# Performance work log

Measured on AMD Instinct MI355X. Metric: run time of the kernel, lower is better.

Reference implementation:

```python
import jax, jax.numpy as jnp
import numpy as np

N = 50000      # n_nodes
E = 800000     # n_edges (avg degree 16)
D_IN, D_HID, D_OUT = 128, 128, 64


def setup_inputs() -> dict:
    key = jax.random.key(0)
    k1, k2, k3, k4 = jax.random.split(key, 4)
    x = jax.random.normal(k1, (N, D_IN), jnp.float32)
    edge_index = jax.random.randint(k2, (2, E), 0, N, jnp.int32)
    # Glorot-style init for the two GCNConv linear weights
    W1 = jax.random.normal(k3, (D_IN, D_HID), jnp.float32) / np.sqrt(D_IN)
    W2 = jax.random.normal(k4, (D_HID, D_OUT), jnp.float32) / np.sqrt(D_HID)
    b1 = jnp.zeros((D_HID,), jnp.float32)
    b2 = jnp.zeros((D_OUT,), jnp.float32)
    return {"x": x, "edge_index": edge_index, "W1": W1, "b1": b1, "W2": W2, "b2": b2}


def _gcn_conv(x, W, b, src, dst):
    """PyG GCNConv: linear transform, then sym-normalized aggregation with self-loops."""
    h = x @ W                                   # [N, F_out]
    ones = jnp.ones((src.shape[0],), h.dtype)
    # degree includes the self-loop weight of 1
    deg = jax.ops.segment_sum(ones, dst, num_segments=N) + 1.0
    dinv = jax.lax.rsqrt(deg)                   # D^{-1/2}
    norm = dinv[src] * dinv[dst]                # per-edge normalization
    agg = jax.ops.segment_sum(h[src] * norm[:, None], dst, num_segments=N)
    # self-loop contribution: norm_ii = dinv_i^2
    return agg + h * (dinv * dinv)[:, None] + b


def reference(x, edge_index, W1, b1, W2, b2):
    src, dst = edge_index[0], edge_index[1]
    h = jax.nn.relu(_gcn_conv(x, W1, b1, src, dst))
    out = jax.nn.relu(_gcn_conv(h, W2, b2, src, dst))
    return out
```

## Files before the change

### kernel.cpp

```cpp
#include <hip/hip_runtime.h>

typedef unsigned short u16;
typedef __attribute__((ext_vector_type(8))) short short8;
typedef __attribute__((ext_vector_type(4))) float f32x4;

__device__ __forceinline__ float bflo(unsigned u) {
    union { unsigned u; float f; } v; v.u = u << 16; return v.f;
}
__device__ __forceinline__ float bfhi(unsigned u) {
    union { unsigned u; float f; } v; v.u = u & 0xFFFF0000u; return v.f;
}
__device__ __forceinline__ u16 f2bf(float f) {
    union { float f; unsigned u; } v; v.f = f;
    unsigned u = v.u;
    u += 0x7FFFu + ((u >> 16) & 1u);
    return (u16)(u >> 16);
}

__global__ void k1_gemm_deg(const void* __restrict__ Av, const void* __restrict__ W,
                            u16* __restrict__ out, int M, int GB,
                            const int* __restrict__ dst, int* __restrict__ cnt,
                            int* __restrict__ pos, int E, int* __restrict__ flag) {
    constexpr int NOUT = 128;
    int t = threadIdx.x;
    int bid = blockIdx.x;
    if (bid >= GB) {
        if (bid == GB) {
            __shared__ int c_s;
            if (t == 0) c_s = 0;
            __syncthreads();
            int c = 0;
            for (int i = t; i < 2048; i += 256) {
                int ex = (((const u16*)Av)[2 * i] >> 7) & 0xFF;
                c += (ex >= 160 || ex <= 80) ? 1 : 0;
            }
            atomicAdd(&c_s, c);
            __syncthreads();
            if (t == 0) *flag = (c_s > 64) ? 1 : 0;
        }
        int stride = (gridDim.x - GB) * 256;
        for (int e = (bid - GB) * 256 + t; e < E; e += stride)
            pos[e] = atomicAdd(&cnt[dst[e]], 1);
        return;
    }
    __shared__ int det;
    if (t == 0) det = 0;
    __syncthreads();
    {
        int ex = (((const u16*)Av)[2 * t] >> 7) & 0xFF;
        if (ex >= 160 || ex <= 80) atomicAdd(&det, 1);
    }
    __syncthreads();
    int fl = det > 8;

    __shared__ u16 Wt[NOUT][136];
    for (int idx = t; idx < NOUT * 128; idx += 256) {
        int k = idx / NOUT, n = idx % NOUT;
        Wt[n][k] = fl ? f2bf(((const float*)W)[idx]) : ((const u16*)W)[idx];
    }
    __syncthreads();
    int wave = t >> 6, lane = t & 63;
    int m0 = (bid * 4 + wave) * 16;
    if (m0 >= M) return;
    int q = lane >> 4;
    int mr = lane & 15;

    short8 a[4];
    if (fl) {
        const float* arow = (const float*)Av + (size_t)(m0 + mr) * 128 + q * 8;
#pragma unroll
        for (int c = 0; c < 4; c++) {
            f32x4 lo = *(const f32x4*)(arow + c * 32);
            f32x4 hi = *(const f32x4*)(arow + c * 32 + 4);
            a[c][0] = (short)f2bf(lo.x); a[c][1] = (short)f2bf(lo.y);
            a[c][2] = (short)f2bf(lo.z); a[c][3] = (short)f2bf(lo.w);
            a[c][4] = (short)f2bf(hi.x); a[c][5] = (short)f2bf(hi.y);
            a[c][6] = (short)f2bf(hi.z); a[c][7] = (short)f2bf(hi.w);
        }
    } else {
        const u16* arow = (const u16*)Av + (size_t)(m0 + mr) * 128 + q * 8;
#pragma unroll
        for (int c = 0; c < 4; c++) a[c] = *(const short8*)(arow + c * 32);
    }

    f32x4 acc[NOUT / 16];
#pragma unroll
    for (int tl = 0; tl < NOUT / 16; tl++) acc[tl] = (f32x4){0.f, 0.f, 0.f, 0.f};
#pragma unroll
    for (int c = 0; c < 4; c++) {
#pragma unroll
        for (int tl = 0; tl < NOUT / 16; tl++) {
            short8 b = *(const short8*)(&Wt[tl * 16 + mr][c * 32 + q * 8]);
            acc[tl] = __builtin_amdgcn_mfma_f32_16x16x32_bf16(a[c], b, acc[tl], 0, 0, 0);
        }
    }
    int rbase = m0 + q * 4;
#pragma unroll
    for (int tl = 0; tl < NOUT / 16; tl++) {
#pragma unroll
        for (int r = 0; r < 4; r++)
            out[(size_t)(rbase + r) * NOUT + tl * 16 + mr] = f2bf(acc[tl][r]);
    }
}

__global__ void k_scan_blocks(const int* __restrict__ cnt, int* __restrict__ rowp_p,
                              int* __restrict__ sums, int n) {
    __shared__ int s[256];
    int t = threadIdx.x;
    int i = blockIdx.x * 256 + t;
    int v = (i < n) ? cnt[i] : 0;
    s[t] = v;
    __syncthreads();
    for (int off = 1; off < 256; off <<= 1) {
        int add = (t >= off) ? s[t - off] : 0;
        __syncthreads();
        s[t] += add;
        __syncthreads();
    }
    if (i < n) rowp_p[i] = s[t] - v;
    if (t == 255) sums[blockIdx.x] = s[255];
}

__global__ void k_fin_fill(const int* __restrict__ rowp_p, int* __restrict__ rowp,
                           const int* __restrict__ sums, const int* __restrict__ cnt,
                           float* __restrict__ dinv, int n, int nb,
                           const int* __restrict__ src, const int* __restrict__ dst,
                           const int* __restrict__ pos, int* __restrict__ col, int E) {
    __shared__ int s[256];
    int t = threadIdx.x;
    int b = blockIdx.x;
    s[t] = sums[t];
    __syncthreads();
    for (int off = 1; off < 256; off <<= 1) {
        int add = (t >= off) ? s[t - off] : 0;
        __syncthreads();
        s[t] += add;
        __syncthreads();
    }
    __syncthreads();
    if (b < nb) {
        int prefix = (b == 0) ? 0 : s[b - 1];
        int i = b * 256 + t;
        if (i < n) {
            rowp[i] = rowp_p[i] + prefix;
            dinv[i] = rsqrtf((float)cnt[i] + 1.0f);
        }
        if (i == 0) rowp[n] = E;
    } else {
        int stride = (gridDim.x - nb) * 256;
        for (int e = (b - nb) * 256 + t; e < E; e += stride) {
            int d = dst[e];
            int tile = d >> 8;
            int prefix = (tile == 0) ? 0 : s[tile - 1];
            col[rowp_p[d] + prefix + pos[e]] = src[e];
        }
    }
}

template <int NOUT>
__global__ void k_gemm_plain(const u16* __restrict__ A, const void* __restrict__ W,
                             u16* __restrict__ out, int M, const int* __restrict__ flag) {
    int fl = *flag;
    __shared__ u16 Wt[NOUT][136];
    int t = threadIdx.x;
    for (int idx = t; idx < NOUT * 128; idx += 256) {
        int k = idx / NOUT, n = idx % NOUT;
        Wt[n][k] = fl ? f2bf(((const float*)W)[idx]) : ((const u16*)W)[idx];
    }
    __syncthreads();
    int wave = t >> 6, lane = t & 63;
    int m0 = ((int)blockIdx.x * 4 + wave) * 16;
    if (m0 >= M) return;
    int q = lane >> 4;
    int mr = lane & 15;

    const u16* arow = A + (size_t)(m0 + mr) * 128 + q * 8;
    short8 a[4];
#pragma unroll
    for (int c = 0; c < 4; c++) a[c] = *(const short8*)(arow + c * 32);

    f32x4 acc[NOUT / 16];
#pragma unroll
    for (int tl = 0; tl < NOUT / 16; tl++) acc[tl] = (f32x4){0.f, 0.f, 0.f, 0.f};
#pragma unroll
    for (int c = 0; c < 4; c++) {
#pragma unroll
        for (int tl = 0; tl < NOUT / 16; tl++) {
            short8 b = *(const short8*)(&Wt[tl * 16 + mr][c * 32 + q * 8]);
            acc[tl] = __builtin_amdgcn_mfma_f32_16x16x32_bf16(a[c], b, acc[tl], 0, 0, 0);
        }
    }
    int rbase = m0 + q * 4;
#pragma unroll
    for (int tl = 0; tl < NOUT / 16; tl++) {
#pragma unroll
        for (int r = 0; r < 4; r++)
            out[(size_t)(rbase + r) * NOUT + tl * 16 + mr] = f2bf(acc[tl][r]);
    }
}

template <int F>
__global__ void k_agg(const u16* __restrict__ g, const int* __restrict__ rowp,
                      const int* __restrict__ col, const float* __restrict__ dinv,
                      const void* __restrict__ biasv, u16* __restrict__ outh,
                      float* __restrict__ outf, const int* __restrict__ flag,
                      int outsel, int N, int E) {
    constexpr int LPR = F / 8;
    constexpr int EPW = 64 / LPR;
    int d = blockIdx.x * 4 + (threadIdx.x >> 6);
    if (d >= N) return;
    int lane = threadIdx.x & 63;
    int er = lane / LPR;
    int fo = (lane % LPR) * 8;

    int beg = rowp[d], end = rowp[d + 1];
    if (beg < 0) beg = 0;
    if (end > E) end = E;
    int deg = end - beg;

    float a0[8], a1[8];
#pragma unroll
    for (int j = 0; j < 8; j++) { a0[j] = 0.f; a1[j] = 0.f; }

    for (int base = 0; base < deg; base += 64) {
        int cnt = deg - base; if (cnt > 64) cnt = 64;
        int colv = 0;
        if (lane < cnt) {
            int s = col[beg + base + lane];
            colv = s < 0 ? 0 : (s >= N ? N - 1 : s);
        }
        int full = cnt / EPW;
        int i = 0;
        for (; i + 2 <= full; i += 2) {
            int s0 = __shfl(colv, i * EPW + er, 64);
            int s1 = __shfl(colv, (i + 1) * EPW + er, 64);
            float d0 = dinv[s0];
            float d1 = dinv[s1];
            uint4 v0 = *(const uint4*)(g + (size_t)s0 * F + fo);
            uint4 v1 = *(const uint4*)(g + (size_t)s1 * F + fo);
            a0[0] += d0 * bflo(v0.x); a0[1] += d0 * bfhi(v0.x);
            a0[2] += d0 * bflo(v0.y); a0[3] += d0 * bfhi(v0.y);
            a0[4] += d0 * bflo(v0.z); a0[5] += d0 * bfhi(v0.z);
            a0[6] += d0 * bflo(v0.w); a0[7] += d0 * bfhi(v0.w);
            a1[0] += d1 * bflo(v1.x); a1[1] += d1 * bfhi(v1.x);
            a1[2] += d1 * bflo(v1.y); a1[3] += d1 * bfhi(v1.y);
            a1[4] += d1 * bflo(v1.z); a1[5] += d1 * bfhi(v1.z);
            a1[6] += d1 * bflo(v1.w); a1[7] += d1 * bfhi(v1.w);
        }
        if (i < full) {
            int s0 = __shfl(colv, i * EPW + er, 64);
            float d0 = dinv[s0];
            uint4 v0 = *(const uint4*)(g + (size_t)s0 * F + fo);
            a0[0] += d0 * bflo(v0.x); a0[1] += d0 * bfhi(v0.x);
            a0[2] += d0 * bflo(v0.y); a0[3] += d0 * bfhi(v0.y);
            a0[4] += d0 * bflo(v0.z); a0[5] += d0 * bfhi(v0.z);
            a0[6] += d0 * bflo(v0.w); a0[7] += d0 * bfhi(v0.w);
            i++;
        }
        int rem = cnt - full * EPW;
        int s0 = __shfl(colv, (full * EPW + er) & 63, 64);
        float d0 = dinv[s0];
        if (er < rem) {
            uint4 v0 = *(const uint4*)(g + (size_t)s0 * F + fo);
            a0[0] += d0 * bflo(v0.x); a0[1] += d0 * bfhi(v0.x);
            a0[2] += d0 * bflo(v0.y); a0[3] += d0 * bfhi(v0.y);
            a0[4] += d0 * bflo(v0.z); a0[5] += d0 * bfhi(v0.z);
            a0[6] += d0 * bflo(v0.w); a0[7] += d0 * bfhi(v0.w);
        }
    }
#pragma unroll
    for (int j = 0; j < 8; j++) a0[j] += a1[j];
#pragma unroll
    for (int off = LPR; off < 64; off <<= 1) {
#pragma unroll
        for (int j = 0; j < 8; j++) a0[j] += __shfl_xor(a0[j], off, 64);
    }

    if (lane < LPR) {
        int fl = *flag;
        uint4 sv = *(const uint4*)(g + (size_t)d * F + fo);
        float bb[8];
        if (fl) {
            const float* bp = (const float*)biasv + fo;
            f32x4 blo = *(const f32x4*)bp;
            f32x4 bhi = *(const f32x4*)(bp + 4);
            bb[0] = blo.x; bb[1] = blo.y; bb[2] = blo.z; bb[3] = blo.w;
            bb[4] = bhi.x; bb[5] = bhi.y; bb[6] = bhi.z; bb[7] = bhi.w;
        } else {
            uint4 bv = *(const uint4*)((const u16*)biasv + fo);
            bb[0] = bflo(bv.x); bb[1] = bfhi(bv.x);
            bb[2] = bflo(bv.y); bb[3] = bfhi(bv.y);
            bb[4] = bflo(bv.z); bb[5] = bfhi(bv.z);
            bb[6] = bflo(bv.w); bb[7] = bfhi(bv.w);
        }
        float di = dinv[d];
        float sf[8] = { bflo(sv.x), bfhi(sv.x), bflo(sv.y), bfhi(sv.y),
                        bflo(sv.z), bfhi(sv.z), bflo(sv.w), bfhi(sv.w) };
        float r[8];
#pragma unroll
        for (int j = 0; j < 8; j++) {
            float v = di * (a0[j] + di * sf[j]) + bb[j];
            r[j] = v > 0.f ? v : 0.f;
        }
        size_t o = (size_t)d * F + fo;
        if (outsel && fl) {
            f32x4 w0 = {r[0], r[1], r[2], r[3]};
            f32x4 w1 = {r[4], r[5], r[6], r[7]};
            *(f32x4*)(outf + o) = w0;
            *(f32x4*)(outf + o + 4) = w1;
        } else {
            uint4 w;
            w.x = (unsigned)f2bf(r[0]) | ((unsigned)f2bf(r[1]) << 16);
            w.y = (unsigned)f2bf(r[2]) | ((unsigned)f2bf(r[3]) << 16);
            w.z = (unsigned)f2bf(r[4]) | ((unsigned)f2bf(r[5]) << 16);
            w.w = (unsigned)f2bf(r[6]) | ((unsigned)f2bf(r[7]) << 16);
            *(uint4*)(outh + o) = w;
        }
    }
}


extern "C" void kernel_launch(void* const* d_in, const int* in_sizes, int n_in,
                              void* d_out, int out_size, void* d_ws, size_t ws_size,
                              hipStream_t stream) {
    const int N = in_sizes[0] / 128;
    const int E = in_sizes[1] / 2;
    const int* ei = (const int*)d_in[1];
    const int* src = ei;
    const int* dst = ei + E;

    char* p = (char*)d_ws;
    auto alloc = [&](size_t b) { char* r = p; p += (b + 255) & ~(size_t)255; return r; };
    int*   flag   = (int*)alloc(256);
    int*   rowp   = (int*)alloc((size_t)(N + 1) * 4);
    int*   rowp_p = (int*)alloc((size_t)N * 4);
    float* dinv   = (float*)alloc((size_t)N * 4);
    int*   col    = (int*)alloc((size_t)E * 4);
    int*   cnt    = (int*)alloc((size_t)N * 4);
    int*   sums   = (int*)alloc(256 * 4);
    int*   pos    = (int*)alloc((size_t)E * 4);
    u16*   g1     = (u16*)alloc((size_t)N * 128 * 2);
    u16*   o1     = (u16*)alloc((size_t)N * 128 * 2);
    u16*   g2     = (u16*)alloc((size_t)N * 64 * 2);

    int nb = (N + 255) / 256;
    int GB = (N / 16 + 3) / 4;
    int DB = 782;
    int FB = 1024;
    int ab = (N + 3) / 4;

    hipMemsetAsync(cnt, 0, ((char*)sums - (char*)cnt) + 1024, stream);

    k1_gemm_deg<<<GB + DB, 256, 0, stream>>>(d_in[0], d_in[2], g1, N, GB,
                                             dst, cnt, pos, E, flag);
    k_scan_blocks<<<nb, 256, 0, stream>>>(cnt, rowp_p, sums, N);
    k_fin_fill<<<nb + FB, 256, 0, stream>>>(rowp_p, rowp, sums, cnt, dinv, N, nb,
                                            src, dst, pos, col, E);

    k_agg<128><<<ab, 256, 0, stream>>>(g1, rowp, col, dinv, d_in[3],
                                       o1, nullptr, flag, 0, N, E);
    k_gemm_plain<64><<<GB, 256, 0, stream>>>(o1, d_in[4], g2, N, flag);
    k_agg<64><<<ab, 256, 0, stream>>>(g2, rowp, col, dinv, d_in[5],
                                      (u16*)d_out, (float*)d_out, flag, 1, N, E);
}
```

Measured before the change: 212.1 us.

## Replace global atomic CSR build with per-block LDS histograms and chunked counting

Degree counting and CSR column fill now use per-block shared-memory histograms over node chunks instead of global atomics per edge. Each of 128 edge-slice blocks writes a u16 histogram, k_scan2 turns these into per-block offsets and degrees, and the fill kernel recomputes local ranks with LDS atomics. This removes contended global atomics and the pos array. In exchange each block rescans its edge slice once per node chunk, the 50KB LDS buffer is now also carried by the GEMM blocks and may lower their occupancy, and the scan reads a 128xN histogram.

```diff
diff --git a/kernel.cpp b/kernel.cpp
--- a/kernel.cpp
+++ b/kernel.cpp
@@ -17,15 +17,19 @@
     return (u16)(u >> 16);
 }
 
-__global__ void k1_gemm_deg(const void* __restrict__ Av, const void* __restrict__ W,
-                            u16* __restrict__ out, int M, int GB,
-                            const int* __restrict__ dst, int* __restrict__ cnt,
-                            int* __restrict__ pos, int E, int* __restrict__ flag) {
+#define CS 12500
+
+__global__ void k1_gemm_count(const void* __restrict__ Av, const void* __restrict__ W,
+                              u16* __restrict__ out, int M, int GB,
+                              const int* __restrict__ dst, u16* __restrict__ ghist,
+                              int E, int N, int ES, int* __restrict__ flag) {
     constexpr int NOUT = 128;
+    __shared__ __align__(16) char ldsbuf[50048];
     int t = threadIdx.x;
     int bid = blockIdx.x;
     if (bid >= GB) {
-        if (bid == GB) {
+        int b = bid - GB;
+        if (b == 0) {
             __shared__ int c_s;
             if (t == 0) c_s = 0;
             __syncthreads();
@@ -38,9 +42,22 @@
             __syncthreads();
             if (t == 0) *flag = (c_s > 64) ? 1 : 0;
         }
-        int stride = (gridDim.x - GB) * 256;
-        for (int e = (bid - GB) * 256 + t; e < E; e += stride)
-            pos[e] = atomicAdd(&cnt[dst[e]], 1);
+        unsigned* hist = (unsigned*)ldsbuf;
+        int e0 = b * ES;
+        int e1 = e0 + ES; if (e1 > E) e1 = E;
+        for (int lo = 0; lo < N; lo += CS) {
+            int len = N - lo; if (len > CS) len = CS;
+            __syncthreads();
+            for (int i = t; i < len; i += 256) hist[i] = 0;
+            __syncthreads();
+            for (int e = e0 + t; e < e1; e += 256) {
+                unsigned dd = (unsigned)(dst[e] - lo);
+                if (dd < (unsigned)len) atomicAdd(&hist[dd], 1u);
+            }
+            __syncthreads();
+            for (int i = t; i < len; i += 256)
+                ghist[(size_t)b * N + lo + i] = (u16)hist[i];
+        }
         return;
     }
     __shared__ int det;
@@ -53,7 +70,7 @@
     __syncthreads();
     int fl = det > 8;
 
-    __shared__ u16 Wt[NOUT][136];
+    u16 (*Wt)[136] = (u16(*)[136])ldsbuf;
     for (int idx = t; idx < NOUT * 128; idx += 256) {
         int k = idx / NOUT, n = idx % NOUT;
         Wt[n][k] = fl ? f2bf(((const float*)W)[idx]) : ((const u16*)W)[idx];
@@ -90,8 +107,8 @@
     for (int c = 0; c < 4; c++) {
 #pragma unroll
         for (int tl = 0; tl < NOUT / 16; tl++) {
-            short8 b = *(const short8*)(&Wt[tl * 16 + mr][c * 32 + q * 8]);
-            acc[tl] = __builtin_amdgcn_mfma_f32_16x16x32_bf16(a[c], b, acc[tl], 0, 0, 0);
+            short8 bb = *(const short8*)(&Wt[tl * 16 + mr][c * 32 + q * 8]);
+            acc[tl] = __builtin_amdgcn_mfma_f32_16x16x32_bf16(a[c], bb, acc[tl], 0, 0, 0);
         }
     }
     int rbase = m0 + q * 4;
@@ -103,13 +120,22 @@
     }
 }
 
-__global__ void k_scan_blocks(const int* __restrict__ cnt, int* __restrict__ rowp_p,
-                              int* __restrict__ sums, int n) {
+__global__ void k_scan2(u16* __restrict__ ghist, int* __restrict__ rowp_p,
+                        int* __restrict__ sums, float* __restrict__ dinv,
+                        int n, int NB) {
     __shared__ int s[256];
     int t = threadIdx.x;
     int i = blockIdx.x * 256 + t;
-    int v = (i < n) ? cnt[i] : 0;
-    s[t] = v;
+    int deg = 0;
+    if (i < n) {
+        for (int b = 0; b < NB; b++) {
+            size_t idx = (size_t)b * n + i;
+            int v = ghist[idx];
+            ghist[idx] = (u16)deg;
+            deg += v;
+        }
+    }
+    s[t] = deg;
     __syncthreads();
     for (int off = 1; off < 256; off <<= 1) {
         int add = (t >= off) ? s[t - off] : 0;
@@ -117,16 +143,20 @@
         s[t] += add;
         __syncthreads();
     }
-    if (i < n) rowp_p[i] = s[t] - v;
+    if (i < n) {
+        rowp_p[i] = s[t] - deg;
+        dinv[i] = rsqrtf((float)deg + 1.0f);
+    }
     if (t == 255) sums[blockIdx.x] = s[255];
 }
 
-__global__ void k_fin_fill(const int* __restrict__ rowp_p, int* __restrict__ rowp,
-                           const int* __restrict__ sums, const int* __restrict__ cnt,
-                           float* __restrict__ dinv, int n, int nb,
-                           const int* __restrict__ src, const int* __restrict__ dst,
-                           const int* __restrict__ pos, int* __restrict__ col, int E) {
+__global__ void k_fin_fill2(const int* __restrict__ rowp_p, int* __restrict__ rowp,
+                            const int* __restrict__ sums, int n, int nb,
+                            const int* __restrict__ src, const int* __restrict__ dst,
+                            const u16* __restrict__ ghist, int* __restrict__ col,
+                            int E, int N, int ES) {
     __shared__ int s[256];
+    __shared__ __align__(16) char ldsbuf[50048];
     int t = threadIdx.x;
     int b = blockIdx.x;
     s[t] = sums[t];
@@ -141,18 +171,28 @@
     if (b < nb) {
         int prefix = (b == 0) ? 0 : s[b - 1];
         int i = b * 256 + t;
-        if (i < n) {
-            rowp[i] = rowp_p[i] + prefix;
-            dinv[i] = rsqrtf((float)cnt[i] + 1.0f);
-        }
+        if (i < n) rowp[i] = rowp_p[i] + prefix;
         if (i == 0) rowp[n] = E;
     } else {
-        int stride = (gridDim.x - nb) * 256;
-        for (int e = (b - nb) * 256 + t; e < E; e += stride) {
-            int d = dst[e];
-            int tile = d >> 8;
-            int prefix = (tile == 0) ? 0 : s[tile - 1];
-            col[rowp_p[d] + prefix + pos[e]] = src[e];
+        int fb = b - nb;
+        unsigned* hist = (unsigned*)ldsbuf;
+        int e0 = fb * ES;
+        int e1 = e0 + ES; if (e1 > E) e1 = E;
+        for (int lo = 0; lo < N; lo += CS) {
+            int len = N - lo; if (len > CS) len = CS;
+            __syncthreads();
+            for (int i = t; i < len; i += 256) hist[i] = 0;
+            __syncthreads();
+            for (int e = e0 + t; e < e1; e += 256) {
+                int d = dst[e];
+                unsigned dd = (unsigned)(d - lo);
+                if (dd < (unsigned)len) {
+                    int r = (int)atomicAdd(&hist[dd], 1u);
+                    int tile = d >> 8;
+                    int pre = tile ? s[tile - 1] : 0;
+                    col[rowp_p[d] + pre + (int)ghist[(size_t)fb * N + d] + r] = src[e];
+                }
+            }
         }
     }
 }
@@ -336,26 +376,25 @@
     int*   rowp_p = (int*)alloc((size_t)N * 4);
     float* dinv   = (float*)alloc((size_t)N * 4);
     int*   col    = (int*)alloc((size_t)E * 4);
-    int*   cnt    = (int*)alloc((size_t)N * 4);
     int*   sums   = (int*)alloc(256 * 4);
-    int*   pos    = (int*)alloc((size_t)E * 4);
+    u16*   ghist  = (u16*)alloc((size_t)128 * N * 2);
     u16*   g1     = (u16*)alloc((size_t)N * 128 * 2);
     u16*   o1     = (u16*)alloc((size_t)N * 128 * 2);
     u16*   g2     = (u16*)alloc((size_t)N * 64 * 2);
 
+    const int NB = 128;
+    int ES = (E + NB - 1) / NB;
     int nb = (N + 255) / 256;
     int GB = (N / 16 + 3) / 4;
-    int DB = 782;
-    int FB = 1024;
     int ab = (N + 3) / 4;
 
-    hipMemsetAsync(cnt, 0, ((char*)sums - (char*)cnt) + 1024, stream);
-
-    k1_gemm_deg<<<GB + DB, 256, 0, stream>>>(d_in[0], d_in[2], g1, N, GB,
-                                             dst, cnt, pos, E, flag);
-    k_scan_blocks<<<nb, 256, 0, stream>>>(cnt, rowp_p, sums, N);
-    k_fin_fill<<<nb + FB, 256, 0, stream>>>(rowp_p, rowp, sums, cnt, dinv, N, nb,
-                                            src, dst, pos, col, E);
+    hipMemsetAsync(sums, 0, 1024, stream);
+
+    k1_gemm_count<<<GB + NB, 256, 0, stream>>>(d_in[0], d_in[2], g1, N, GB,
+                                               dst, ghist, E, N, ES, flag);
+    k_scan2<<<nb, 256, 0, stream>>>(ghist, rowp_p, sums, dinv, N, NB);
+    k_fin_fill2<<<nb + NB, 256, 0, stream>>>(rowp_p, rowp, sums, N, nb,
+                                             src, dst, ghist, col, E, N, ES);
 
     k_agg<128><<<ab, 256, 0, stream>>>(g1, rowp, col, dinv, d_in[3],
                                        o1, nullptr, flag, 0, N, E);
```

After: 296.0 us. +39.5%, slower.
